# Kernel tuning notes

Measured on AMD Instinct MI355X. Metric: run time of the kernel, lower is better.

Reference implementation:

```python
import jax, jax.numpy as jnp
import numpy as np

HEADS = 4  # from init_kwargs

def setup_inputs() -> dict:
    key = jax.random.key(0)
    ks = jax.random.split(key, 11)
    B, N, T, E = 1, 16, 2048, 64
    D = E // HEADS
    return {
        "value": jax.random.normal(ks[0], (B, N, T, E), jnp.float32),
        "key":   jax.random.normal(ks[1], (B, N, T, E), jnp.float32),
        "query": jax.random.normal(ks[2], (B, N, T, E), jnp.float32),
        "Wq": jax.random.normal(ks[3], (D, D), jnp.float32) / np.sqrt(D),
        "bq": jax.random.normal(ks[4], (D,), jnp.float32) * 0.01,
        "Wk": jax.random.normal(ks[5], (D, D), jnp.float32) / np.sqrt(D),
        "bk": jax.random.normal(ks[6], (D,), jnp.float32) * 0.01,
        "Wv": jax.random.normal(ks[7], (D, D), jnp.float32) / np.sqrt(D),
        "bv": jax.random.normal(ks[8], (D,), jnp.float32) * 0.01,
        "Wfc": jax.random.normal(ks[9], (E, E), jnp.float32) / np.sqrt(E),
        "bfc": jax.random.normal(ks[10], (E,), jnp.float32) * 0.01,
    }

def reference(value, key, query, Wq, bq, Wk, bk, Wv, bv, Wfc, bfc):
    B, N, T, E = query.shape
    H = HEADS
    D = E // H
    # split heads: [B,N,T,H,D]
    q = query.reshape(B, N, T, H, D) @ Wq + bq
    k = key.reshape(B, N, T, H, D) @ Wk + bk
    v = value.reshape(B, N, T, H, D) @ Wv + bv
    # full score tensor [B,N,Tq,Tk,H]
    scores = jnp.einsum('bnqhd,bnkhd->bnqkh', q, k)
    # NOTE: original softmaxes over dim=2, i.e. the QUERY axis (faithful to source)
    attn = jax.nn.softmax(scores / jnp.float32(E) ** 0.5, axis=2)
    out = jnp.einsum('bnqkh,bnkhd->bnqhd', attn, v).reshape(B, N, T, E)
    return out @ Wfc + bfc
```

## Files before the change

kernel.cpp:

```cpp
#include <hip/hip_runtime.h>

#define N_ 16
#define T_ 2048
#define E_ 64
#define H_ 4
#define D_ 16
#define NH_ 64
#define SEXP_ 0.18033688f

typedef __attribute__((ext_vector_type(4))) _Float16 h4;
typedef __attribute__((ext_vector_type(8))) _Float16 h8;
typedef __attribute__((ext_vector_type(2))) __fp16 g2;
typedef __attribute__((ext_vector_type(4))) float f4;

#if __has_builtin(__builtin_amdgcn_exp2f)
__device__ inline float fast_exp2(float x) { return __builtin_amdgcn_exp2f(x); }
#else
__device__ inline float fast_exp2(float x) {
    float r; asm("v_exp_f32 %0, %1" : "=v"(r) : "v"(x)); return r;
}
#endif

__device__ inline h4 pack4_f16(float a, float b, float c, float d) {
    union { g2 g[2]; h4 h; } u;
    u.g[0] = __builtin_amdgcn_cvt_pkrtz(a, b);
    u.g[1] = __builtin_amdgcn_cvt_pkrtz(c, d);
    return u.h;
}

__global__ __launch_bounds__(256) void proj_kernel(
    const float* __restrict__ xq, const float* __restrict__ Wq, const float* __restrict__ bq,
    const float* __restrict__ xk, const float* __restrict__ Wk, const float* __restrict__ bk,
    const float* __restrict__ xv, const float* __restrict__ Wv, const float* __restrict__ bv,
    const float* __restrict__ Wfc,
    _Float16* __restrict__ Qh, _Float16* __restrict__ Kh, _Float16* __restrict__ Vt,
    _Float16* __restrict__ Wt)
{
    int tid = threadIdx.x;
    int y = blockIdx.y;
    if (y == 3) {
        if (blockIdx.x < 16) {
            int k = blockIdx.x * 4 + (tid >> 6);
            int e = tid & 63;
            Wt[e * 64 + k] = (_Float16)Wfc[k * 64 + e];
        }
        return;
    }
    const float* x = (y == 0) ? xq : (y == 1) ? xk : xv;
    const float* W = (y == 0) ? Wq : (y == 1) ? Wk : Wv;
    const float* b = (y == 0) ? bq : (y == 1) ? bk : bv;
    const float sc = (y == 0) ? SEXP_ : 1.0f;

    __shared__ float Wl[D_ * D_];
    __shared__ float bl[D_];
    Wl[tid] = W[tid];
    if (tid < D_) bl[tid] = b[tid];
    __syncthreads();

    int r = blockIdx.x * 256 + tid;
    int h, t, n;
    if (y == 2) {
        t = r & (T_ - 1);
        h = (r >> 11) & (H_ - 1);
        n = r >> 13;
    } else {
        h = r & (H_ - 1);
        t = (r >> 2) & (T_ - 1);
        n = r >> 13;
    }

    const float4* xp4 = reinterpret_cast<const float4*>(
        x + ((size_t)(n * T_ + t) * E_ + h * D_));
    float xv_[D_];
#pragma unroll
    for (int i = 0; i < 4; i++) {
        float4 v = xp4[i];
        xv_[4*i] = v.x; xv_[4*i+1] = v.y; xv_[4*i+2] = v.z; xv_[4*i+3] = v.w;
    }
    float acc[D_];
#pragma unroll
    for (int i = 0; i < D_; i++) acc[i] = bl[i];
#pragma unroll
    for (int j = 0; j < D_; j++) {
        float xj = xv_[j];
#pragma unroll
        for (int i = 0; i < D_; i++) acc[i] = fmaf(xj, Wl[j * D_ + i], acc[i]);
    }
    if (y == 2) {
        _Float16* vb = Vt + (size_t)(n * H_ + h) * D_ * T_ + t;
#pragma unroll
        for (int d = 0; d < D_; d++) vb[(size_t)d * T_] = (_Float16)acc[d];
    } else {
        _Float16 ob[16];
#pragma unroll
        for (int i = 0; i < D_; i++) ob[i] = (_Float16)(acc[i] * sc);
        _Float16* o = (y == 0) ? Qh : Kh;
        uint4* dst = reinterpret_cast<uint4*>(o + (size_t)((n * H_ + h) * T_ + t) * D_);
        dst[0] = reinterpret_cast<uint4*>(ob)[0];
        dst[1] = reinterpret_cast<uint4*>(ob)[1];
    }
}

__global__ __launch_bounds__(256) void stats_kernel(
    const _Float16* __restrict__ Qh, const _Float16* __restrict__ Kh,
    float* __restrict__ Lp)
{
    int tid = threadIdx.x;
    int lane = tid & 63, wave = tid >> 6;
    int row = lane & 15, quad = lane >> 4;
    int nh = blockIdx.x;
    int kt0 = (blockIdx.y * 4 + wave) * 4;
    int z = blockIdx.z;
    const _Float16* Kb = Kh + (size_t)nh * T_ * D_;
    const _Float16* Qb = Qh + (size_t)nh * T_ * D_;

    h4 a[4];
#pragma unroll
    for (int j = 0; j < 4; j++)
        a[j] = *reinterpret_cast<const h4*>(Kb + ((kt0 + j) * 16 + row) * D_ + quad * 4);

    f4 l[4];
#pragma unroll
    for (int j = 0; j < 4; j++) l[j] = (f4){0.f, 0.f, 0.f, 0.f};
    f4 z4 = {0.f, 0.f, 0.f, 0.f};

    int q_lo = z * (T_ / 4), q_hi = q_lo + T_ / 4;
#pragma unroll 4
    for (int q0 = q_lo; q0 < q_hi; q0 += 16) {
        h4 b = *reinterpret_cast<const h4*>(Qb + (q0 + row) * D_ + quad * 4);
#pragma unroll
        for (int j = 0; j < 4; j++) {
            f4 s = __builtin_amdgcn_mfma_f32_16x16x16f16(a[j], b, z4, 0, 0, 0);
#pragma unroll
            for (int i = 0; i < 4; i++) l[j][i] += fast_exp2(s[i]);
        }
    }
#pragma unroll
    for (int off = 1; off < 16; off <<= 1)
#pragma unroll
        for (int j = 0; j < 4; j++)
#pragma unroll
            for (int i = 0; i < 4; i++)
                l[j][i] += __shfl_xor(l[j][i], off, 64);

    if (row == 0) {
        float* lp = Lp + ((size_t)z * NH_ + nh) * T_;
#pragma unroll
        for (int j = 0; j < 4; j++)
            *reinterpret_cast<f4*>(lp + (kt0 + j) * 16 + quad * 4) = l[j];
    }
}

__global__ __launch_bounds__(256) void attn_kernel(
    const _Float16* __restrict__ Qh, const _Float16* __restrict__ Kh,
    const _Float16* __restrict__ Vt, const float* __restrict__ Lp,
    float* __restrict__ PO)
{
    __shared__ __align__(16) _Float16 rlh[512];
    int tid = threadIdx.x;
    int lane = tid & 63, wave = tid >> 6;
    int row = lane & 15, quad = lane >> 4;
    int nh = blockIdx.x;
    int qt0 = (blockIdx.y * 4 + wave) * 4;
    int z = blockIdx.z;
    int k_lo = z * (T_ / 4);

    {
        int kk = tid * 2;
        float s0 = 0.f, s1 = 0.f;
#pragma unroll
        for (int zz = 0; zz < 4; zz++) {
            float2 lv = *reinterpret_cast<const float2*>(
                Lp + ((size_t)zz * NH_ + nh) * T_ + k_lo + kk);
            s0 += lv.x; s1 += lv.y;
        }
        g2 pk = __builtin_amdgcn_cvt_pkrtz(1.0f / s0, 1.0f / s1);
        *reinterpret_cast<g2*>(&rlh[kk]) = pk;
    }
    __syncthreads();

    const _Float16* Kb = Kh + (size_t)nh * T_ * D_;
    const _Float16* Qb = Qh + (size_t)nh * T_ * D_;
    const _Float16* Vb = Vt + (size_t)nh * D_ * T_ + (size_t)row * T_;

    h4 b[4];
#pragma unroll
    for (int j = 0; j < 4; j++)
        b[j] = *reinterpret_cast<const h4*>(Qb + ((qt0 + j) * 16 + row) * D_ + quad * 4);

    f4 o[4];
#pragma unroll
    for (int j = 0; j < 4; j++) o[j] = (f4){0.f, 0.f, 0.f, 0.f};
    f4 z4 = {0.f, 0.f, 0.f, 0.f};

    int pr = ((row & 12) << 1) | (row & 3);

    int k_hi = k_lo + T_ / 4;
#pragma unroll 2
    for (int k0 = k_lo; k0 < k_hi; k0 += 32) {
        h4 a0 = *reinterpret_cast<const h4*>(Kb + (k0 + pr) * D_ + quad * 4);
        h4 a1 = *reinterpret_cast<const h4*>(Kb + (k0 + pr + 4) * D_ + quad * 4);
        h8 v = *reinterpret_cast<const h8*>(Vb + k0 + quad * 8);
        h8 rv = *reinterpret_cast<const h8*>(&rlh[(k0 - k_lo) + quad * 8]);
        v = v * rv;
#pragma unroll
        for (int j = 0; j < 4; j++) {
            f4 s0 = __builtin_amdgcn_mfma_f32_16x16x16f16(a0, b[j], z4, 0, 0, 0);
            f4 s1 = __builtin_amdgcn_mfma_f32_16x16x16f16(a1, b[j], z4, 0, 0, 0);
            union { h4 h[2]; h8 h8v; } p;
            p.h[0] = pack4_f16(fast_exp2(s0[0]), fast_exp2(s0[1]),
                               fast_exp2(s0[2]), fast_exp2(s0[3]));
            p.h[1] = pack4_f16(fast_exp2(s1[0]), fast_exp2(s1[1]),
                               fast_exp2(s1[2]), fast_exp2(s1[3]));
            o[j] = __builtin_amdgcn_mfma_f32_16x16x32_f16(p.h8v, v, o[j], 0, 0, 0);
        }
    }
    int n = nh >> 2, h = nh & 3;
    float* po = PO + (size_t)z * N_ * T_ * E_ + (size_t)n * T_ * E_ + h * D_ + row;
#pragma unroll
    for (int j = 0; j < 4; j++)
#pragma unroll
        for (int i = 0; i < 4; i++) {
            int q0 = (qt0 + j) * 16 + quad * 4 + i;
            po[(size_t)q0 * E_] = o[j][i];
        }
}

__global__ __launch_bounds__(256) void fc_kernel(
    const float* __restrict__ PO, const _Float16* __restrict__ Wt,
    const float* __restrict__ bfc, float* __restrict__ out)
{
    int tid = threadIdx.x;
    int lane = tid & 63, wave = tid >> 6;
    int row = lane & 15, quad = lane >> 4;
    int g = blockIdx.x * 4 + wave;
    int r0 = g * 16;
    size_t base = (size_t)(r0 + row) * E_;
    const size_t zstride = (size_t)N_ * T_ * E_ / 4;

    h8 a[2];
#pragma unroll
    for (int half = 0; half < 2; half++) {
        f4 u0 = {0.f,0.f,0.f,0.f}, u1 = {0.f,0.f,0.f,0.f};
#pragma unroll
        for (int zz = 0; zz < 4; zz++) {
            const f4* p = reinterpret_cast<const f4*>(PO) + zz * zstride + base / 4;
            f4 w0 = p[half * 8 + quad * 2];
            f4 w1 = p[half * 8 + quad * 2 + 1];
#pragma unroll
            for (int i = 0; i < 4; i++) { u0[i] += w0[i]; u1[i] += w1[i]; }
        }
        union { h4 h[2]; h8 v; } pk;
        pk.h[0] = pack4_f16(u0[0], u0[1], u0[2], u0[3]);
        pk.h[1] = pack4_f16(u1[0], u1[1], u1[2], u1[3]);
        a[half] = pk.v;
    }
    f4 acc[4];
#pragma unroll
    for (int ne = 0; ne < 4; ne++) {
        const _Float16* wtb = Wt + (size_t)(ne * 16 + row) * 64;
        h8 b0 = *reinterpret_cast<const h8*>(wtb + quad * 8);
        h8 b1 = *reinterpret_cast<const h8*>(wtb + 32 + quad * 8);
        acc[ne] = __builtin_amdgcn_mfma_f32_16x16x32_f16(a[0], b0, (f4){0.f,0.f,0.f,0.f}, 0, 0, 0);
        acc[ne] = __builtin_amdgcn_mfma_f32_16x16x32_f16(a[1], b1, acc[ne], 0, 0, 0);
    }
#pragma unroll
    for (int ne = 0; ne < 4; ne++) {
        float bias = bfc[ne * 16 + row];
#pragma unroll
        for (int i = 0; i < 4; i++)
            out[(size_t)(r0 + quad * 4 + i) * E_ + ne * 16 + row] = acc[ne][i] + bias;
    }
}

extern "C" void kernel_launch(void* const* d_in, const int* in_sizes, int n_in,
                              void* d_out, int out_size, void* d_ws, size_t ws_size,
                              hipStream_t stream) {
    (void)in_sizes; (void)n_in; (void)out_size; (void)ws_size;
    const float* value = (const float*)d_in[0];
    const float* key   = (const float*)d_in[1];
    const float* query = (const float*)d_in[2];
    const float* Wq    = (const float*)d_in[3];
    const float* bq    = (const float*)d_in[4];
    const float* Wk    = (const float*)d_in[5];
    const float* bk    = (const float*)d_in[6];
    const float* Wv    = (const float*)d_in[7];
    const float* bv    = (const float*)d_in[8];
    const float* Wfc   = (const float*)d_in[9];
    const float* bfc   = (const float*)d_in[10];
    float* out = (float*)d_out;

    char* ws = (char*)d_ws;
    _Float16* Qh  = (_Float16*)(ws);
    _Float16* Kh  = (_Float16*)(ws + (4u << 20));
    _Float16* Vt  = (_Float16*)(ws + (8u << 20));
    _Float16* Wt  = (_Float16*)(ws + (12u << 20));
    float*    Lp  = (float*)   (ws + (13u << 20));
    float*    PO  = (float*)   (ws + (15u << 20));

    proj_kernel<<<dim3(512, 4), 256, 0, stream>>>(
        query, Wq, bq, key, Wk, bk, value, Wv, bv, Wfc, Qh, Kh, Vt, Wt);
    stats_kernel<<<dim3(NH_, 8, 4), 256, 0, stream>>>(Qh, Kh, Lp);
    attn_kernel<<<dim3(NH_, 8, 4), 256, 0, stream>>>(Qh, Kh, Vt, Lp, PO);
    fc_kernel<<<512, 256, 0, stream>>>(PO, Wt, bfc, out);
}
```

Before: 175.5 us.

## Fuse softmax column-sum stats into attention kernel with block-wide query coverage

Replaces the separate stats and attention kernels with one kernel where each 1024-thread block covers all 2048 queries for a key chunk. Because the softmax runs over the query axis, each key's normaliser can then be built inside the block by shared-memory atomics on per-chunk partial sums. This removes the second pass that recomputes QK^T and exp, plus the Lp round-trip through global memory. In exchange it adds a block barrier per 32-key step, triple-buffered LDS sums, a prefetch of the next K/V, and higher register pressure from 8 query tiles per wave, with only 256 blocks in the grid.

```diff
diff --git a/kernel.cpp b/kernel.cpp
--- a/kernel.cpp
+++ b/kernel.cpp
@@ -18,6 +18,14 @@
 #else
 __device__ inline float fast_exp2(float x) {
     float r; asm("v_exp_f32 %0, %1" : "=v"(r) : "v"(x)); return r;
+}
+#endif
+
+#if __has_builtin(__builtin_amdgcn_rcpf)
+__device__ inline float fast_rcp(float x) { return __builtin_amdgcn_rcpf(x); }
+#else
+__device__ inline float fast_rcp(float x) {
+    float r; asm("v_rcp_f32 %0, %1" : "=v"(r) : "v"(x)); return r;
 }
 #endif
 
@@ -101,127 +109,108 @@
     }
 }
 
-__global__ __launch_bounds__(256) void stats_kernel(
+__global__ __launch_bounds__(1024) void fused_attn_kernel(
     const _Float16* __restrict__ Qh, const _Float16* __restrict__ Kh,
-    float* __restrict__ Lp)
+    const _Float16* __restrict__ Vt, float* __restrict__ PO)
 {
+    __shared__ __align__(16) float l[3][32];
     int tid = threadIdx.x;
     int lane = tid & 63, wave = tid >> 6;
     int row = lane & 15, quad = lane >> 4;
     int nh = blockIdx.x;
-    int kt0 = (blockIdx.y * 4 + wave) * 4;
-    int z = blockIdx.z;
-    const _Float16* Kb = Kh + (size_t)nh * T_ * D_;
-    const _Float16* Qb = Qh + (size_t)nh * T_ * D_;
-
-    h4 a[4];
-#pragma unroll
-    for (int j = 0; j < 4; j++)
-        a[j] = *reinterpret_cast<const h4*>(Kb + ((kt0 + j) * 16 + row) * D_ + quad * 4);
-
-    f4 l[4];
-#pragma unroll
-    for (int j = 0; j < 4; j++) l[j] = (f4){0.f, 0.f, 0.f, 0.f};
-    f4 z4 = {0.f, 0.f, 0.f, 0.f};
-
-    int q_lo = z * (T_ / 4), q_hi = q_lo + T_ / 4;
-#pragma unroll 4
-    for (int q0 = q_lo; q0 < q_hi; q0 += 16) {
-        h4 b = *reinterpret_cast<const h4*>(Qb + (q0 + row) * D_ + quad * 4);
-#pragma unroll
-        for (int j = 0; j < 4; j++) {
-            f4 s = __builtin_amdgcn_mfma_f32_16x16x16f16(a[j], b, z4, 0, 0, 0);
-#pragma unroll
-            for (int i = 0; i < 4; i++) l[j][i] += fast_exp2(s[i]);
-        }
-    }
-#pragma unroll
-    for (int off = 1; off < 16; off <<= 1)
-#pragma unroll
-        for (int j = 0; j < 4; j++)
-#pragma unroll
-            for (int i = 0; i < 4; i++)
-                l[j][i] += __shfl_xor(l[j][i], off, 64);
-
-    if (row == 0) {
-        float* lp = Lp + ((size_t)z * NH_ + nh) * T_;
-#pragma unroll
-        for (int j = 0; j < 4; j++)
-            *reinterpret_cast<f4*>(lp + (kt0 + j) * 16 + quad * 4) = l[j];
-    }
-}
-
-__global__ __launch_bounds__(256) void attn_kernel(
-    const _Float16* __restrict__ Qh, const _Float16* __restrict__ Kh,
-    const _Float16* __restrict__ Vt, const float* __restrict__ Lp,
-    float* __restrict__ PO)
-{
-    __shared__ __align__(16) _Float16 rlh[512];
-    int tid = threadIdx.x;
-    int lane = tid & 63, wave = tid >> 6;
-    int row = lane & 15, quad = lane >> 4;
-    int nh = blockIdx.x;
-    int qt0 = (blockIdx.y * 4 + wave) * 4;
-    int z = blockIdx.z;
+    int z = blockIdx.y;
     int k_lo = z * (T_ / 4);
 
-    {
-        int kk = tid * 2;
-        float s0 = 0.f, s1 = 0.f;
-#pragma unroll
-        for (int zz = 0; zz < 4; zz++) {
-            float2 lv = *reinterpret_cast<const float2*>(
-                Lp + ((size_t)zz * NH_ + nh) * T_ + k_lo + kk);
-            s0 += lv.x; s1 += lv.y;
-        }
-        g2 pk = __builtin_amdgcn_cvt_pkrtz(1.0f / s0, 1.0f / s1);
-        *reinterpret_cast<g2*>(&rlh[kk]) = pk;
-    }
-    __syncthreads();
+    if (tid < 96) ((float*)l)[tid] = 0.f;
 
     const _Float16* Kb = Kh + (size_t)nh * T_ * D_;
     const _Float16* Qb = Qh + (size_t)nh * T_ * D_;
     const _Float16* Vb = Vt + (size_t)nh * D_ * T_ + (size_t)row * T_;
 
-    h4 b[4];
-#pragma unroll
-    for (int j = 0; j < 4; j++)
-        b[j] = *reinterpret_cast<const h4*>(Qb + ((qt0 + j) * 16 + row) * D_ + quad * 4);
-
-    f4 o[4];
-#pragma unroll
-    for (int j = 0; j < 4; j++) o[j] = (f4){0.f, 0.f, 0.f, 0.f};
+    h4 b[8];
+#pragma unroll
+    for (int j = 0; j < 8; j++)
+        b[j] = *reinterpret_cast<const h4*>(Qb + ((wave * 8 + j) * 16 + row) * D_ + quad * 4);
+
+    f4 o[8];
+#pragma unroll
+    for (int j = 0; j < 8; j++) o[j] = (f4){0.f, 0.f, 0.f, 0.f};
     f4 z4 = {0.f, 0.f, 0.f, 0.f};
 
     int pr = ((row & 12) << 1) | (row & 3);
 
-    int k_hi = k_lo + T_ / 4;
-#pragma unroll 2
-    for (int k0 = k_lo; k0 < k_hi; k0 += 32) {
-        h4 a0 = *reinterpret_cast<const h4*>(Kb + (k0 + pr) * D_ + quad * 4);
-        h4 a1 = *reinterpret_cast<const h4*>(Kb + (k0 + pr + 4) * D_ + quad * 4);
-        h8 v = *reinterpret_cast<const h8*>(Vb + k0 + quad * 8);
-        h8 rv = *reinterpret_cast<const h8*>(&rlh[(k0 - k_lo) + quad * 8]);
-        v = v * rv;
-#pragma unroll
-        for (int j = 0; j < 4; j++) {
+    h4 a0 = *reinterpret_cast<const h4*>(Kb + (k_lo + pr) * D_ + quad * 4);
+    h4 a1 = *reinterpret_cast<const h4*>(Kb + (k_lo + pr + 4) * D_ + quad * 4);
+    h8 v  = *reinterpret_cast<const h8*>(Vb + k_lo + quad * 8);
+
+    __syncthreads();
+
+    int cur = 0;
+    for (int c = 0; c < 16; c++) {
+        int k0 = k_lo + c * 32;
+        h8 p[8];
+        float lp[8];
+#pragma unroll
+        for (int t = 0; t < 8; t++) lp[t] = 0.f;
+
+#pragma unroll
+        for (int j = 0; j < 8; j++) {
             f4 s0 = __builtin_amdgcn_mfma_f32_16x16x16f16(a0, b[j], z4, 0, 0, 0);
             f4 s1 = __builtin_amdgcn_mfma_f32_16x16x16f16(a1, b[j], z4, 0, 0, 0);
-            union { h4 h[2]; h8 h8v; } p;
-            p.h[0] = pack4_f16(fast_exp2(s0[0]), fast_exp2(s0[1]),
-                               fast_exp2(s0[2]), fast_exp2(s0[3]));
-            p.h[1] = pack4_f16(fast_exp2(s1[0]), fast_exp2(s1[1]),
-                               fast_exp2(s1[2]), fast_exp2(s1[3]));
-            o[j] = __builtin_amdgcn_mfma_f32_16x16x32_f16(p.h8v, v, o[j], 0, 0, 0);
-        }
-    }
+            float e0 = fast_exp2(s0[0]), e1 = fast_exp2(s0[1]),
+                  e2 = fast_exp2(s0[2]), e3 = fast_exp2(s0[3]);
+            float e4 = fast_exp2(s1[0]), e5 = fast_exp2(s1[1]),
+                  e6 = fast_exp2(s1[2]), e7 = fast_exp2(s1[3]);
+            lp[0] += e0; lp[1] += e1; lp[2] += e2; lp[3] += e3;
+            lp[4] += e4; lp[5] += e5; lp[6] += e6; lp[7] += e7;
+            union { h4 h[2]; h8 h8v; } pk;
+            pk.h[0] = pack4_f16(e0, e1, e2, e3);
+            pk.h[1] = pack4_f16(e4, e5, e6, e7);
+            p[j] = pk.h8v;
+        }
+
+        int kn = (c == 15) ? k_lo : k0 + 32;
+        h4 na0 = *reinterpret_cast<const h4*>(Kb + (kn + pr) * D_ + quad * 4);
+        h4 na1 = *reinterpret_cast<const h4*>(Kb + (kn + pr + 4) * D_ + quad * 4);
+        h8 nv  = *reinterpret_cast<const h8*>(Vb + kn + quad * 8);
+
+#pragma unroll
+        for (int off = 1; off < 16; off <<= 1)
+#pragma unroll
+            for (int t = 0; t < 8; t++) lp[t] += __shfl_xor(lp[t], off, 64);
+        if (row == 0) {
+#pragma unroll
+            for (int t = 0; t < 8; t++) atomicAdd(&l[cur][quad * 8 + t], lp[t]);
+        }
+        __syncthreads();
+
+        int zb = cur + 2; if (zb >= 3) zb -= 3;
+        if (wave == 0 && lane < 32) l[zb][lane] = 0.f;
+
+        f4 la = *reinterpret_cast<f4*>(&l[cur][quad * 8]);
+        f4 lb = *reinterpret_cast<f4*>(&l[cur][quad * 8 + 4]);
+        union { h4 h[2]; h8 h8v; } rk;
+        rk.h[0] = pack4_f16(fast_rcp(la[0]), fast_rcp(la[1]),
+                            fast_rcp(la[2]), fast_rcp(la[3]));
+        rk.h[1] = pack4_f16(fast_rcp(lb[0]), fast_rcp(lb[1]),
+                            fast_rcp(lb[2]), fast_rcp(lb[3]));
+        h8 vs = v * rk.h8v;
+
+#pragma unroll
+        for (int j = 0; j < 8; j++)
+            o[j] = __builtin_amdgcn_mfma_f32_16x16x32_f16(p[j], vs, o[j], 0, 0, 0);
+
+        a0 = na0; a1 = na1; v = nv;
+        cur = cur + 1; if (cur >= 3) cur -= 3;
+    }
+
     int n = nh >> 2, h = nh & 3;
     float* po = PO + (size_t)z * N_ * T_ * E_ + (size_t)n * T_ * E_ + h * D_ + row;
 #pragma unroll
-    for (int j = 0; j < 4; j++)
+    for (int j = 0; j < 8; j++)
 #pragma unroll
         for (int i = 0; i < 4; i++) {
-            int q0 = (qt0 + j) * 16 + quad * 4 + i;
+            int q0 = (wave * 8 + j) * 16 + quad * 4 + i;
             po[(size_t)q0 * E_] = o[j][i];
         }
 }
@@ -295,12 +284,10 @@
     _Float16* Kh  = (_Float16*)(ws + (4u << 20));
     _Float16* Vt  = (_Float16*)(ws + (8u << 20));
     _Float16* Wt  = (_Float16*)(ws + (12u << 20));
-    float*    Lp  = (float*)   (ws + (13u << 20));
     float*    PO  = (float*)   (ws + (15u << 20));
 
     proj_kernel<<<dim3(512, 4), 256, 0, stream>>>(
         query, Wq, bq, key, Wk, bk, value, Wv, bv, Wfc, Qh, Kh, Vt, Wt);
-    stats_kernel<<<dim3(NH_, 8, 4), 256, 0, stream>>>(Qh, Kh, Lp);
-    attn_kernel<<<dim3(NH_, 8, 4), 256, 0, stream>>>(Qh, Kh, Vt, Lp, PO);
+    fused_attn_kernel<<<dim3(NH_, 4), 1024, 0, stream>>>(Qh, Kh, Vt, PO);
     fc_kernel<<<512, 256, 0, stream>>>(PO, Wt, bfc, out);
 }
```

New measurement: 219.0 us. 24.8% more time.
